# Optimization experiments

Measured on AMD Instinct MI355X. Metric: run time of the kernel, lower is better.

The kernel has to match this reference:

```python
import jax, jax.numpy as jnp
import numpy as np

NAMES = ['tempo', 'chord', 'barbeat', 'type', 'pitch', 'duration', 'velocity']
VOCABS = [56, 135, 18, 4, 87, 18, 25]
EMBS = [128, 256, 64, 32, 512, 128, 128]
B, S, D, H, L, FF = 2, 2048, 512, 8, 8, 2048
HD = D // H
EPS = 1e-6


def _layernorm(x, g, b):
    m = x.mean(-1, keepdims=True)
    v = ((x - m) ** 2).mean(-1, keepdims=True)
    return (x - m) / jnp.sqrt(v + 1e-5) * g + b


def _rope(x, cos, sin):
    x1, x2 = jnp.split(x, 2, -1)
    return x * cos + jnp.concatenate([-x2, x1], -1) * sin


def _causal_linear_attn(q, k, v):
    # kernelized causal linear attention: phi = elu + 1, cumulative-sum normalization
    q = jax.nn.elu(q) + 1.0
    k = jax.nn.elu(k) + 1.0
    kv = jnp.cumsum(jnp.einsum('bshd,bshm->bshdm', k, v), axis=1)  # [B,S,H,HD,HD]
    z = 1.0 / (jnp.einsum('bshd,bshd->bsh', q, jnp.cumsum(k, axis=1)) + EPS)
    return jnp.einsum('bshd,bshdm->bshm', q, kv) * z[..., None]


def _forward(inputs, target, emb_tables, in_W, in_b, Wq, bq, Wk, bk, Wv, bv, Wo, bo,
             ln1_g, ln1_b, ln2_g, ln2_b, W1, b1, W2, b2, norm_g, norm_b, pWs, pbs, catW, catb):
    # multi-field embedding, each scaled by sqrt(d_emb) (CPEmbedding)
    embs = [emb_tables[i][inputs[..., i]] * jnp.sqrt(jnp.float32(EMBS[i])) for i in range(7)]
    x = jnp.concatenate(embs, -1) @ in_W + in_b  # [B,S,D]
    # PositionalEncoding: original indexes pe at position seq_len -> single d_model vector
    div = jnp.exp(jnp.arange(0, D, 2, dtype=jnp.float32) * (-np.log(10000.0) / D))
    pe = jnp.zeros((D,), jnp.float32).at[0::2].set(jnp.sin(S * div)).at[1::2].set(jnp.cos(S * div))
    x = x + pe
    # rotary tables for head_dim
    inv_freq = 1.0 / (10000.0 ** (jnp.arange(0, HD, 2, dtype=jnp.float32) / HD))
    fr = jnp.arange(S, dtype=jnp.float32)[:, None] * inv_freq[None, :]
    ang = jnp.concatenate([fr, fr], -1)  # [S,HD]
    cos = jnp.cos(ang)[None, :, None, :]
    sin = jnp.sin(ang)[None, :, None, :]
    for l in range(L):
        q = (x @ Wq[l] + bq[l]).reshape(B, S, H, HD)
        k = (x @ Wk[l] + bk[l]).reshape(B, S, H, HD)
        v = (x @ Wv[l] + bv[l]).reshape(B, S, H, HD)
        q = _rope(q, cos, sin)
        k = _rope(k, cos, sin)
        a = _causal_linear_attn(q, k, v).reshape(B, S, D) @ Wo[l] + bo[l]
        x = x + a
        y = x = _layernorm(x, ln1_g[l], ln1_b[l])
        y = jax.nn.gelu(y @ W1[l] + b1[l], approximate=False) @ W2[l] + b2[l]
        x = _layernorm(x + y, ln2_g[l], ln2_b[l])
    x = _layernorm(x, norm_g, norm_b)
    # MultiProj with teacher-forced type embedding (target branch)
    emb_t = emb_tables[3][target[..., 3]] * jnp.sqrt(jnp.float32(EMBS[3]))
    proj_type = (x @ pWs[3] + pbs[3]) * jnp.sqrt(jnp.float32(VOCABS[3]))  # from pre-concat x
    xc = jnp.concatenate([x, emb_t], -1) @ catW + catb
    outs = []
    for i in range(7):
        if i == 3:
            outs.append(proj_type)
        else:
            outs.append((xc @ pWs[i] + pbs[i]) * jnp.sqrt(jnp.float32(VOCABS[i])))
    return jnp.concatenate(outs, -1)  # [B,S,sum(VOCABS)=343]


def setup_inputs():
    key = jax.random.key(0)
    kit = iter(jax.random.split(key, 64))
    s = 0.02
    d = {}
    d['inputs'] = jax.random.randint(next(kit), (B, S, 7), 0, 4)
    d['target'] = jax.random.randint(next(kit), (B, S, 7), 0, 4)
    for i, n in enumerate(NAMES):
        d['emb_' + n] = jax.random.normal(next(kit), (VOCABS[i], EMBS[i]), jnp.float32) * s
    E = sum(EMBS)
    d['in_W'] = jax.random.normal(next(kit), (E, D)) * s
    d['in_b'] = jnp.zeros((D,))
    for nm, sh in [('Wq', (L, D, D)), ('Wk', (L, D, D)), ('Wv', (L, D, D)), ('Wo', (L, D, D)), ('W1', (L, D, FF)), ('W2', (L, FF, D))]:
        d[nm] = jax.random.normal(next(kit), sh) * s
    for nm, sh in [('bq', (L, D)), ('bk', (L, D)), ('bv', (L, D)), ('bo', (L, D)), ('b1', (L, FF)), ('b2', (L, D)), ('ln1_b', (L, D)), ('ln2_b', (L, D)), ('norm_b', (D,)), ('catb', (D,))]:
        d[nm] = jnp.zeros(sh)
    d['ln1_g'] = jnp.ones((L, D))
    d['ln2_g'] = jnp.ones((L, D))
    d['norm_g'] = jnp.ones((D,))
    for i, n in enumerate(NAMES):
        d['pW_' + n] = jax.random.normal(next(kit), (D, VOCABS[i])) * s
        d['pb_' + n] = jnp.zeros((VOCABS[i],))
    d['catW'] = jax.random.normal(next(kit), (D + 32, D)) * s
    return d


def reference(inputs, target, emb_tempo, emb_chord, emb_barbeat, emb_type, emb_pitch, emb_duration, emb_velocity,
              in_W, in_b, Wq, bq, Wk, bk, Wv, bv, Wo, bo, ln1_g, ln1_b, ln2_g, ln2_b, W1, b1, W2, b2,
              norm_g, norm_b, pW_tempo, pb_tempo, pW_chord, pb_chord, pW_barbeat, pb_barbeat, pW_type, pb_type,
              pW_pitch, pb_pitch, pW_duration, pb_duration, pW_velocity, pb_velocity, catW, catb):
    emb_tables = [emb_tempo, emb_chord, emb_barbeat, emb_type, emb_pitch, emb_duration, emb_velocity]
    pWs = [pW_tempo, pW_chord, pW_barbeat, pW_type, pW_pitch, pW_duration, pW_velocity]
    pbs = [pb_tempo, pb_chord, pb_barbeat, pb_type, pb_pitch, pb_duration, pb_velocity]
    return _forward(inputs, target, emb_tables, in_W, in_b, Wq, bq, Wk, bk, Wv, bv, Wo, bo,
                    ln1_g, ln1_b, ln2_g, ln2_b, W1, b1, W2, b2, norm_g, norm_b, pWs, pbs, catW, catb)
```

## Files before the change

### kernel.cpp

```cpp
#include <hip/hip_runtime.h>
#include <math.h>

typedef unsigned short u16;
typedef short bf16x8 __attribute__((ext_vector_type(8)));
typedef float f32x4 __attribute__((ext_vector_type(4)));
typedef u16 u16x4 __attribute__((ext_vector_type(4)));
typedef u16 u16x8 __attribute__((ext_vector_type(8)));

#define NB 2
#define NS 2048
#define ND 512
#define NH 8
#define NHD 64
#define NL 8
#define NFF 2048
#define NM (NB*NS)
#define NE 1248
#define NEP 1280
#define NXC 576
#define CHK 64
#define NCH (NS/CHK)
#define QKVW 1536

__device__ inline float b2f(u16 u){ union{ unsigned int i; float f;} x; x.i = ((unsigned int)u)<<16; return x.f; }
__device__ inline u16 f2b(float f){ union{ float f; unsigned int i;} x; x.f=f; unsigned int r = x.i + 0x7fffu + ((x.i>>16)&1u); return (u16)(r>>16); }

__global__ void k_embed(const int* __restrict__ inp,
    const float* __restrict__ e0, const float* __restrict__ e1, const float* __restrict__ e2,
    const float* __restrict__ e3, const float* __restrict__ e4, const float* __restrict__ e5,
    const float* __restrict__ e6, u16* __restrict__ xe)
{
  int row = blockIdx.x;
  int i0 = inp[row*7+0], i1 = inp[row*7+1], i2 = inp[row*7+2], i3 = inp[row*7+3],
      i4 = inp[row*7+4], i5 = inp[row*7+5], i6 = inp[row*7+6];
  size_t base = (size_t)row*NEP;
  for (int c = threadIdx.x; c < NEP; c += 256){
    float val = 0.f;
    if      (c < 128)  val = e0[i0*128 + c]        * 11.3137084990f;
    else if (c < 384)  val = e1[i1*256 + (c-128)]  * 16.0f;
    else if (c < 448)  val = e2[i2*64  + (c-384)]  * 8.0f;
    else if (c < 480)  val = e3[i3*32  + (c-448)]  * 5.6568542495f;
    else if (c < 992)  val = e4[i4*512 + (c-480)]  * 22.6274169980f;
    else if (c < 1120) val = e5[i5*128 + (c-992)]  * 11.3137084990f;
    else if (c < NE)   val = e6[i6*128 + (c-1120)] * 11.3137084990f;
    xe[base + c] = f2b(val);
  }
}

__device__ inline void trans_tile(const float* __restrict__ W, u16* __restrict__ WT,
                                  int K, int N, int Kpad, int bx, int by){
  __shared__ float t[32][33];
  int tx = threadIdx.x & 31, ty = threadIdx.x >> 5;
  int k0 = by*32, n0 = bx*32;
  #pragma unroll
  for (int i=0;i<4;i++){
    int k = k0 + ty + i*8, n = n0 + tx;
    t[ty+i*8][tx] = (k<K && n<N) ? W[(size_t)k*N + n] : 0.f;
  }
  __syncthreads();
  #pragma unroll
  for (int i=0;i<4;i++){
    int n = n0 + ty + i*8, k = k0 + tx;
    if (n<N && k<Kpad) WT[(size_t)n*Kpad + k] = f2b(t[tx][ty+i*8]);
  }
}

__global__ void k_prepw(const float* __restrict__ Wq, const float* __restrict__ Wk,
                        const float* __restrict__ Wv, const float* __restrict__ Wo,
                        const float* __restrict__ in_W, const float* __restrict__ catW,
                        const float* __restrict__ W1, const float* __restrict__ W2,
                        u16* __restrict__ qkvoT, u16* __restrict__ inWT, u16* __restrict__ catWT,
                        u16* __restrict__ w1T, u16* __restrict__ w2T)
{
  int bid = blockIdx.x;
  if (bid < 8192){
    int z = bid >> 8, r = bid & 255;
    int l = z >> 2, s2 = z & 3;
    const float* W = (s2==0?Wq:s2==1?Wk:s2==2?Wv:Wo) + (size_t)l*ND*ND;
    trans_tile(W, qkvoT + (size_t)z*ND*ND, ND, ND, ND, r & 15, r >> 4);
  } else if (bid < 8832){
    int r = bid - 8192;
    trans_tile(in_W, inWT, NE, ND, NEP, r & 15, r >> 4);
  } else if (bid < 9120){
    int r = bid - 8832;
    trans_tile(catW, catWT, 544, ND, NXC, r & 15, r >> 4);
  } else {
    int r = bid - 9120;
    int l = r >> 11; int b2 = r & 2047;
    if (b2 < 1024) trans_tile(W1 + (size_t)l*ND*NFF, w1T + (size_t)l*ND*NFF, ND, NFF, ND, b2 & 63, b2 >> 6);
    else { b2 -= 1024; trans_tile(W2 + (size_t)l*NFF*ND, w2T + (size_t)l*NFF*ND, NFF, ND, NFF, b2 & 15, b2 >> 4); }
  }
}

__global__ void k_misc(float* __restrict__ rc, float* __restrict__ rs,
    const float* p0,const float* p1,const float* p2,const float* p3,
    const float* p4,const float* p5,const float* p6,
    const float* q0,const float* q1,const float* q2,const float* q3,
    const float* q4,const float* q5,const float* q6,
    u16* __restrict__ pwcT, float* __restrict__ pbc,
    u16* __restrict__ ptT, float* __restrict__ pbt,
    const float* __restrict__ bq, const float* __restrict__ bk, const float* __restrict__ bv,
    float* __restrict__ bqkv, const float* __restrict__ in_b, float* __restrict__ bias_in)
{
  int idx = blockIdx.x*256 + threadIdx.x;
  if (idx < NS*32){
    int s = idx >> 5, j = idx & 31;
    double inv = exp(-(double)(2*j) * log(10000.0) / (double)NHD);
    double ang = (double)s * inv;
    rc[idx] = (float)cos(ang);
    rs[idx] = (float)sin(ang);
  }
  const int off[8] = {0,56,191,209,213,300,318,343};
  {
    int col = idx >> 9, k = idx & 511;
    if (col < 384){
      u16 v = 0;
      if (col < 343){
        int f = 0;
        while (col >= off[f+1]) f++;
        int cc = col - off[f];
        int V = off[f+1]-off[f];
        const float* P = (f==0)?p0:(f==1)?p1:(f==2)?p2:(f==3)?p3:(f==4)?p4:(f==5)?p5:p6;
        v = f2b(P[(size_t)k*V + cc] * sqrtf((float)V));
      }
      pwcT[(size_t)col*512 + k] = v;
    }
    if (idx < 64*512){
      int n = idx >> 9;
      ptT[idx] = (n < 4) ? f2b(p3[(size_t)k*4 + n]*2.0f) : (u16)0;
    }
  }
  if (idx < 343){
    int c2 = idx, f = 0;
    while (c2 >= off[f+1]) f++;
    int cc = c2 - off[f]; int V = off[f+1]-off[f];
    const float* Q = (f==0)?q0:(f==1)?q1:(f==2)?q2:(f==3)?q3:(f==4)?q4:(f==5)?q5:q6;
    pbc[idx] = Q[cc]*sqrtf((float)V);
  }
  if (idx < 4) pbt[idx] = q3[idx]*2.0f;
  if (idx < NL*QKVW){
    int l = idx / QKVW, c = idx % QKVW;
    float v = (c < 512) ? bq[l*512 + c] : (c < 1024) ? bk[l*512 + c - 512] : bv[l*512 + c - 1024];
    bqkv[idx] = v;
  }
  if (idx < ND){
    double div = exp(-(double)(idx & ~1) * log(10000.0) / (double)ND);
    double ang = (double)NS * div;
    float pev = (idx & 1) ? (float)cos(ang) : (float)sin(ang);
    bias_in[idx] = in_b[idx] + pev;
  }
}

template<int ACT, int NT, int TM>
__global__ __launch_bounds__(256) void k_gemm(
    const u16* __restrict__ A, const u16* __restrict__ BT,
    const float* __restrict__ bias, float* __restrict__ Cf, u16* __restrict__ Cb,
    int N, int klen, int lda, int ldb, int ldc,
    int koff, float* __restrict__ Cf2,
    const float* __restrict__ rc, const float* __restrict__ rs)
{
  constexpr int MREP = TM/32;
  __shared__ u16 SH[TM*64 + NT*32*64];
  u16* As = SH;
  u16* Bs = SH + TM*64;
  int tid = threadIdx.x;
  int w = tid >> 6, lane = tid & 63;

  int kz = blockIdx.z;
  A  += (size_t)kz*koff;
  BT += (size_t)kz*koff;
  if (kz){ Cf = Cf2; bias = nullptr; }

  int nwg = gridDim.x*gridDim.y;
  int d = blockIdx.y*gridDim.x + blockIdx.x;
  int wl = ((nwg & 7) == 0) ? ((d & 7)*(nwg >> 3) + (d >> 3)) : d;
  int bx = wl % gridDim.x, by = wl / gridDim.x;
  int m0 = by*TM, n0 = bx*(NT*32);

  f32x4 acc[MREP][NT];
  #pragma unroll
  for (int m=0;m<MREP;m++)
    #pragma unroll
    for (int n=0;n<NT;n++) acc[m][n] = (f32x4){0.f,0.f,0.f,0.f};

  int lg = lane>>3;
  int cg = (lane&7) ^ lg;
  const u16* ag = A  + (size_t)(m0 + w*(TM/4) + lg)*lda + cg*8;
  const u16* bg = BT + (size_t)(n0 + w*(NT*8) + lg)*ldb + cg*8;
  int wr = (w>>1)*(TM/2), wc = (w&1)*(NT*16);
  int lr = lane & 15;
  int rx = lr & 7;
  int cb_ = lane >> 4;
  int g = lane >> 4;

  int nk = klen >> 6;
  for (int t = 0; t < nk; ++t){
    int k0 = t << 6;
    #pragma unroll
    for (int i=0;i<TM/32;i++)
      __builtin_amdgcn_global_load_lds(
        (__attribute__((address_space(1))) void*)(void*)(ag + (size_t)(i*8)*lda + k0),
        (__attribute__((address_space(3))) void*)(&As[(w*(TM/4) + i*8)*64]), 16, 0, 0);
    #pragma unroll
    for (int j=0;j<NT;j++)
      __builtin_amdgcn_global_load_lds(
        (__attribute__((address_space(1))) void*)(void*)(bg + (size_t)(j*8)*ldb + k0),
        (__attribute__((address_space(3))) void*)(&Bs[(w*(NT*8) + j*8)*64]), 16, 0, 0);
    __syncthreads();
    #pragma unroll
    for (int kk=0;kk<2;kk++){
      int gA = ((kk*4 + cb_) ^ rx) * 8;
      bf16x8 af[MREP], bfr[NT];
      #pragma unroll
      for (int m=0;m<MREP;m++) af[m]  = *(const bf16x8*)&As[(wr + m*16 + lr)*64 + gA];
      #pragma unroll
      for (int n=0;n<NT;n++)   bfr[n] = *(const bf16x8*)&Bs[(wc + n*16 + lr)*64 + gA];
      #pragma unroll
      for (int m=0;m<MREP;m++)
        #pragma unroll
        for (int n=0;n<NT;n++)
          acc[m][n] = __builtin_amdgcn_mfma_f32_16x16x32_bf16(af[m], bfr[n], acc[m][n], 0,0,0);
    }
    __syncthreads();
  }

  if (ACT == 2){
    float* Cs = (float*)SH;
    #pragma unroll
    for (int n=0;n<NT;n++){
      int col = wc + n*16 + lr;
      float bv = bias ? bias[n0 + col] : 0.f;
      #pragma unroll
      for (int m=0;m<MREP;m++)
        #pragma unroll
        for (int r=0;r<4;r++)
          Cs[(wr + m*16 + g*4 + r)*64 + col] = acc[m][n][r] + bv;
    }
    __syncthreads();
    if (n0 < 1024){
      #pragma unroll
      for (int i=0;i<8;i++){
        int p = tid + i*256;
        int row = p >> 5, j = p & 31;
        float a1 = Cs[row*64 + j], a2 = Cs[row*64 + j + 32];
        int s = (m0 + row) & (NS-1);
        float c = rc[s*32+j], sn = rs[s*32+j];
        float r1 = a1*c - a2*sn, r2 = a2*c + a1*sn;
        Cb[(size_t)(m0+row)*ldc + n0 + j]      = f2b((r1 > 0.f) ? r1+1.f : expf(r1));
        Cb[(size_t)(m0+row)*ldc + n0 + j + 32] = f2b((r2 > 0.f) ? r2+1.f : expf(r2));
      }
    } else {
      #pragma unroll
      for (int i=0;i<16;i++){
        int p = tid + i*256;
        int row = p >> 6, c2 = p & 63;
        Cb[(size_t)(m0+row)*ldc + n0 + c2] = f2b(Cs[row*64 + c2]);
      }
    }
    return;
  }

  #pragma unroll
  for (int n=0;n<NT;n++){
    int col = n0 + wc + n*16 + lr;
    if (col < N){
      float bv = bias ? bias[col] : 0.f;
      #pragma unroll
      for (int m=0;m<MREP;m++){
        #pragma unroll
        for (int r=0;r<4;r++){
          int row = m0 + wr + m*16 + g*4 + r;
          float v = acc[m][n][r] + bv;
          if (ACT==1) v = 0.5f*v*(1.f+erff(v*0.70710678118654752f));
          if (Cf) Cf[(size_t)row*ldc + col] = v;
          if (Cb) Cb[(size_t)row*ldc + col] = f2b(v);
        }
      }
    }
  }
}

__global__ __launch_bounds__(256) void k_att1(const u16* __restrict__ qkv, float* __restrict__ pref){
  int c = blockIdx.x, h = blockIdx.y, b = blockIdx.z;
  __shared__ u16 Kt[64*64];
  __shared__ u16 Vt[80*64];
  int tid = threadIdx.x;
  {
    int t = tid & 63, dseg = (tid>>6)*16;
    const u16* kg = qkv + ((size_t)(b*NS + c*CHK + t))*QKVW + 512 + h*NHD + dseg;
    u16x8 k0 = *(const u16x8*)kg;
    u16x8 k1 = *(const u16x8*)(kg+8);
    u16x8 v0 = *(const u16x8*)(kg+512);
    u16x8 v1 = *(const u16x8*)(kg+520);
    #pragma unroll
    for (int e=0;e<8;e++){
      int d0 = dseg+e, d1 = dseg+8+e;
      Kt[(d0*64+t) ^ ((d0&7)<<3)] = k0[e];
      Kt[(d1*64+t) ^ ((d1&7)<<3)] = k1[e];
      Vt[(d0*64+t) ^ ((d0&7)<<3)] = v0[e];
      Vt[(d1*64+t) ^ ((d1&7)<<3)] = v1[e];
    }
    if (tid < 64) Vt[4096 + tid] = 0x3F80;
    for (int e = tid; e < 15*64; e += 256){
      int r = 65 + (e>>6), tt = e&63;
      Vt[(r*64+tt) ^ ((r&7)<<3)] = 0;
    }
  }
  __syncthreads();
  int lane = tid & 63, w = tid >> 6;
  int lr = lane & 15, lk = (lane>>4)*8;
  f32x4 acc[5];
  #pragma unroll
  for (int i=0;i<5;i++) acc[i] = (f32x4){0.f,0.f,0.f,0.f};
  #pragma unroll
  for (int kk=0;kk<2;kk++){
    int mcol = w*16 + lr;
    bf16x8 bfrag = *(const bf16x8*)&Kt[(mcol*64 + kk*32 + lk) ^ ((mcol&7)<<3)];
    #pragma unroll
    for (int fr=0; fr<5; fr++){
      int arow = fr*16 + lr;
      bf16x8 afrag = *(const bf16x8*)&Vt[(arow*64 + kk*32 + lk) ^ ((arow&7)<<3)];
      acc[fr] = __builtin_amdgcn_mfma_f32_16x16x32_bf16(afrag, bfrag, acc[fr], 0,0,0);
    }
  }
  size_t base = (((size_t)(b*NH + h))*NCH + c)*5120;
  int g = lane>>4;
  #pragma unroll
  for (int fr=0; fr<5; fr++)
    #pragma unroll
    for (int r=0;r<4;r++)
      pref[base + (fr*16 + g*4 + r)*64 + w*16 + lr] = acc[fr][r];
}

__global__ __launch_bounds__(256) void k_att2(float* __restrict__ pref){
  int bh = blockIdx.y;
  int e = blockIdx.x*256 + threadIdx.x;
  size_t base = (size_t)bh*NCH*5120 + e;
  float v[NCH];
  #pragma unroll
  for (int c=0;c<NCH;c++) v[c] = pref[base + (size_t)c*5120];
  float run = 0.f;
  #pragma unroll
  for (int c=0;c<NCH;c++){ float t = v[c]; pref[base + (size_t)c*5120] = run; run += t; }
}

__global__ __launch_bounds__(256) void k_att3(const u16* __restrict__ qkv,
    const float* __restrict__ pref, u16* __restrict__ outa)
{
  int c = blockIdx.x, h = blockIdx.y, b = blockIdx.z;
  __shared__ u16 Qs[4096], Ks[4096];
  __shared__ u16 Vt[5120], Ps[5120];
  __shared__ float dens[64];
  u16* Sm = Ks;
  int tid = threadIdx.x;
  {
    int row = tid>>2, seg = (tid&3)*16;
    const u16* qg = qkv + ((size_t)(b*NS + c*CHK + row))*QKVW + h*NHD + seg;
    u16x8 q0 = *(const u16x8*)qg;
    u16x8 q1 = *(const u16x8*)(qg+8);
    u16x8 kk0 = *(const u16x8*)(qg+512);
    u16x8 kk1 = *(const u16x8*)(qg+520);
    int sw = (row&7)<<3;
    *(u16x8*)&Qs[(row*64+seg) ^ sw]     = q0;
    *(u16x8*)&Qs[(row*64+seg+8) ^ sw]   = q1;
    *(u16x8*)&Ks[(row*64+seg) ^ sw]     = kk0;
    *(u16x8*)&Ks[(row*64+seg+8) ^ sw]   = kk1;
  }
  {
    int t = tid&63, dseg = (tid>>6)*16;
    const u16* vg = qkv + ((size_t)(b*NS + c*CHK + t))*QKVW + 1024 + h*NHD + dseg;
    u16x8 v0 = *(const u16x8*)vg;
    u16x8 v1 = *(const u16x8*)(vg+8);
    #pragma unroll
    for (int e=0;e<8;e++){
      int d0=dseg+e, d1=dseg+8+e;
      Vt[(d0*64+t)^((d0&7)<<3)] = v0[e];
      Vt[(d1*64+t)^((d1&7)<<3)] = v1[e];
    }
    if (tid<64) Vt[4096+tid] = 0x3F80;
    for (int e=tid; e<15*64; e+=256){
      int r = 65+(e>>6), tt = e&63;
      Vt[(r*64+tt)^((r&7)<<3)] = 0;
    }
  }
  {
    size_t pb = (((size_t)(b*NH + h))*NCH + c)*5120;
    for (int e=tid; e<5120; e+=256){
      int row = e>>6, m = e&63;
      Ps[(row*64+m)^((row&7)<<3)] = f2b(pref[pb+e]);
    }
  }
  __syncthreads();
  int lane = tid&63, w = tid>>6;
  int lr = lane&15, lk = (lane>>4)*8, g = lane>>4;
  f32x4 sacc[4];
  #pragma unroll
  for (int i=0;i<4;i++) sacc[i] = (f32x4){0.f,0.f,0.f,0.f};
  int iq = w*16 + lr;
  #pragma unroll
  for (int kk=0;kk<2;kk++){
    bf16x8 bq = *(const bf16x8*)&Qs[(iq*64 + kk*32 + lk) ^ ((iq&7)<<3)];
    #pragma unroll
    for (int ft=0; ft<4; ft++){
      int tr = ft*16 + lr;
      bf16x8 ak = *(const bf16x8*)&Ks[(tr*64 + kk*32 + lk) ^ ((tr&7)<<3)];
      sacc[ft] = __builtin_amdgcn_mfma_f32_16x16x32_bf16(ak, bq, sacc[ft], 0,0,0);
    }
  }
  __syncthreads();
  #pragma unroll
  for (int ft=0; ft<4; ft++){
    int t0 = ft*16 + g*4;
    u16x4 pk;
    #pragma unroll
    for (int r=0;r<4;r++) pk[r] = f2b((t0+r <= iq) ? sacc[ft][r] : 0.f);
    *(u16x4*)&Sm[(iq*64 + t0) ^ ((iq&7)<<3)] = pk;
  }
  __syncthreads();
  f32x4 acc[5];
  #pragma unroll
  for (int i=0;i<5;i++) acc[i] = (f32x4){0.f,0.f,0.f,0.f};
  #pragma unroll
  for (int kk=0;kk<2;kk++){
    int sw = (iq&7)<<3;
    bf16x8 as = *(const bf16x8*)&Sm[(iq*64 + kk*32 + lk) ^ sw];
    bf16x8 aq = *(const bf16x8*)&Qs[(iq*64 + kk*32 + lk) ^ sw];
    #pragma unroll
    for (int c5=0;c5<5;c5++){
      int col = c5*16 + lr, sw2 = (col&7)<<3;
      bf16x8 bv = *(const bf16x8*)&Vt[(col*64 + kk*32 + lk) ^ sw2];
      bf16x8 bp = *(const bf16x8*)&Ps[(col*64 + kk*32 + lk) ^ sw2];
      acc[c5] = __builtin_amdgcn_mfma_f32_16x16x32_bf16(as, bv, acc[c5], 0,0,0);
      acc[c5] = __builtin_amdgcn_mfma_f32_16x16x32_bf16(aq, bp, acc[c5], 0,0,0);
    }
  }
  if (lr == 0){
    #pragma unroll
    for (int r=0;r<4;r++) dens[w*16 + g*4 + r] = acc[4][r];
  }
  __syncthreads();
  #pragma unroll
  for (int c5=0;c5<4;c5++){
    #pragma unroll
    for (int r=0;r<4;r++){
      int i = w*16 + g*4 + r;
      float z = 1.f/(dens[i] + 1e-6f);
      outa[((size_t)(b*NS + c*CHK + i))*ND + h*NHD + c5*16 + lr] = f2b(acc[c5][r]*z);
    }
  }
}

__global__ __launch_bounds__(256) void k_ln(const float* __restrict__ xin, const float* __restrict__ res,
    const float* __restrict__ res2, float* __restrict__ outx, u16* __restrict__ outb,
    const float* __restrict__ g, const float* __restrict__ bvec,
    const int* __restrict__ tgt, const float* __restrict__ embt, u16* __restrict__ xcb)
{
  int row = blockIdx.x, tid = threadIdx.x;
  size_t base = (size_t)row*ND;
  float v0 = xin[base+tid], v1 = xin[base+tid+256];
  if (res){ v0 += res[base+tid]; v1 += res[base+tid+256]; }
  if (res2){ v0 += res2[base+tid]; v1 += res2[base+tid+256]; }
  float s = v0+v1, ss2 = v0*v0 + v1*v1;
  #pragma unroll
  for (int o = 32; o >= 1; o >>= 1){
    s   += __shfl_down(s, o, 64);
    ss2 += __shfl_down(ss2, o, 64);
  }
  __shared__ float red[8];
  int wv = tid >> 6, ln = tid & 63;
  if (ln == 0){ red[wv] = s; red[4+wv] = ss2; }
  __syncthreads();
  float stot  = red[0]+red[1]+red[2]+red[3];
  float sstot = red[4]+red[5]+red[6]+red[7];
  float mean = stot * (1.0f/ND);
  float var  = sstot * (1.0f/ND) - mean*mean;
  float inv = 1.0f / sqrtf(var + 1e-5f);
  float o0 = (v0-mean)*inv*g[tid]     + bvec[tid];
  float o1 = (v1-mean)*inv*g[tid+256] + bvec[tid+256];
  outx[base+tid] = o0; outx[base+tid+256] = o1;
  if (outb){ outb[base+tid] = f2b(o0); outb[base+tid+256] = f2b(o1); }
  if (xcb){
    size_t xbse = (size_t)row*NXC;
    xcb[xbse+tid] = f2b(o0);
    xcb[xbse+tid+256] = f2b(o1);
    if (tid < 32){
      int id = tgt[row*7+3];
      xcb[xbse+512+tid] = f2b(embt[id*32+tid]*5.6568542495f);
      xcb[xbse+544+tid] = 0;
    }
  }
}

extern "C" void kernel_launch(void* const* d_in, const int* in_sizes, int n_in,
                              void* d_out, int out_size, void* d_ws, size_t ws_size,
                              hipStream_t stream)
{
  const int* inputs = (const int*)d_in[0];
  const int* target = (const int*)d_in[1];
  const float* emb[7];
  for (int i=0;i<7;i++) emb[i] = (const float*)d_in[2+i];
  const float* in_W  = (const float*)d_in[9];
  const float* in_b  = (const float*)d_in[10];
  const float* Wq = (const float*)d_in[11];
  const float* Wk = (const float*)d_in[12];
  const float* Wv = (const float*)d_in[13];
  const float* Wo = (const float*)d_in[14];
  const float* W1 = (const float*)d_in[15];
  const float* W2 = (const float*)d_in[16];
  const float* bq = (const float*)d_in[17];
  const float* bk = (const float*)d_in[18];
  const float* bv = (const float*)d_in[19];
  const float* bo = (const float*)d_in[20];
  const float* b1 = (const float*)d_in[21];
  const float* b2 = (const float*)d_in[22];
  const float* ln1_b = (const float*)d_in[23];
  const float* ln2_b = (const float*)d_in[24];
  const float* norm_b = (const float*)d_in[25];
  const float* catb   = (const float*)d_in[26];
  const float* ln1_g = (const float*)d_in[27];
  const float* ln2_g = (const float*)d_in[28];
  const float* norm_g = (const float*)d_in[29];
  const float* pW[7]; const float* pb[7];
  for (int i=0;i<7;i++){ pW[i]=(const float*)d_in[30+2*i]; pb[i]=(const float*)d_in[31+2*i]; }
  const float* catW = (const float*)d_in[44];
  float* outp = (float*)d_out;

  char* base = (char*)d_ws;
  size_t off = 0;
  auto alloc = [&](size_t bytes)->void*{ void* p = base + off; off += bytes; off = (off + 255) & ~(size_t)255; return p; };

  float* x    = (float*)alloc((size_t)NM*ND*4);
  u16*   xb   = (u16*)  alloc((size_t)NM*ND*2);
  u16*   qkvb = (u16*)  alloc((size_t)NM*QKVW*2);
  float* tb   = (float*)alloc((size_t)NM*ND*4);
  float* tb2  = (float*)alloc((size_t)NM*ND*4);
  u16*   ab   = (u16*)  alloc((size_t)NM*ND*2);
  u16*   hb   = (u16*)  alloc((size_t)NM*NFF*2);
  float* rc   = (float*)alloc((size_t)NS*32*4);
  float* rs   = (float*)alloc((size_t)NS*32*4);
  float* pref = (float*)alloc((size_t)NB*NH*NCH*5120*4);
  u16*  qkvoT = (u16*)  alloc((size_t)NL*4*ND*ND*2);
  u16*  w1T   = (u16*)  alloc((size_t)NL*NFF*ND*2);
  u16*  w2T   = (u16*)  alloc((size_t)NL*ND*NFF*2);
  u16*  inWT  = (u16*)  alloc((size_t)ND*NEP*2);
  u16*  catWT = (u16*)  alloc((size_t)ND*NXC*2);
  u16*  pwcT  = (u16*)  alloc((size_t)384*512*2);
  float* pbc  = (float*)alloc(344*4);
  u16*  ptT   = (u16*)  alloc((size_t)64*512*2);
  float* pbt  = (float*)alloc(4*4);
  float* bqkv = (float*)alloc((size_t)NL*QKVW*4);
  float* bias_in = (float*)alloc(ND*4);
  u16*  xeb = hb;
  u16*  xcb = hb;
  u16*  ocb = hb + (size_t)NM*NXC;

  k_prepw<<<25504, 256, 0, stream>>>(Wq, Wk, Wv, Wo, in_W, catW, W1, W2,
                                     qkvoT, inWT, catWT, w1T, w2T);
  k_misc<<<768, 256, 0, stream>>>(rc, rs,
      pW[0],pW[1],pW[2],pW[3],pW[4],pW[5],pW[6],
      pb[0],pb[1],pb[2],pb[3],pb[4],pb[5],pb[6],
      pwcT, pbc, ptT, pbt, bq, bk, bv, bqkv, in_b, bias_in);

  k_embed<<<NM, 256, 0, stream>>>(inputs, emb[0],emb[1],emb[2],emb[3],emb[4],emb[5],emb[6], xeb);
  k_gemm<0,2,64><<<dim3(8,64,1), 256, 0, stream>>>(xeb, inWT, bias_in, x, xb,
      ND, NEP, NEP, NEP, ND, 0, nullptr, nullptr, nullptr);

  dim3 agrid(NCH, NH, NB);
  for (int l = 0; l < NL; l++){
    const u16* woT = qkvoT + (size_t)(l*4+3)*ND*ND;
    k_gemm<2,2,64><<<dim3(24,64,1), 256, 0, stream>>>(xb, qkvoT + (size_t)l*4*ND*ND,
        bqkv + l*QKVW, nullptr, qkvb, QKVW, ND, ND, ND, QKVW, 0, nullptr, rc, rs);
    k_att1<<<agrid, 256, 0, stream>>>(qkvb, pref);
    k_att2<<<dim3(20,16), 256, 0, stream>>>(pref);
    k_att3<<<agrid, 256, 0, stream>>>(qkvb, pref, ab);
    k_gemm<0,2,64><<<dim3(8,64,2), 256, 0, stream>>>(ab, woT, bo + l*ND, tb, nullptr,
        ND, 256, ND, ND, ND, 256, tb2, nullptr, nullptr);
    k_ln<<<NM, 256, 0, stream>>>(x, tb, tb2, x, xb, ln1_g + l*ND, ln1_b + l*ND,
                                 nullptr, nullptr, nullptr);
    k_gemm<1,2,64><<<dim3(32,64,1), 256, 0, stream>>>(xb, w1T + (size_t)l*NFF*ND,
        b1 + l*NFF, nullptr, hb, NFF, ND, ND, ND, NFF, 0, nullptr, nullptr, nullptr);
    k_gemm<0,2,64><<<dim3(8,64,2), 256, 0, stream>>>(hb, w2T + (size_t)l*ND*NFF,
        b2 + l*ND, tb, nullptr, ND, 1024, NFF, NFF, ND, 1024, tb2, nullptr, nullptr);
    k_ln<<<NM, 256, 0, stream>>>(x, tb, tb2, x, xb, ln2_g + l*ND, ln2_b + l*ND,
                                 nullptr, nullptr, nullptr);
  }

  k_ln<<<NM, 256, 0, stream>>>(x, nullptr, nullptr, x, xb, norm_g, norm_b,
                               target, emb[3], xcb);

  k_gemm<0,2,64><<<dim3(8,64,1), 256, 0, stream>>>(xcb, catWT, catb, nullptr, ocb,
      ND, NXC, NXC, NXC, ND, 0, nullptr, nullptr, nullptr);
  k_gemm<0,2,64><<<dim3(6,64,1), 256, 0, stream>>>(ocb, pwcT, pbc, outp, nullptr,
      343, ND, ND, ND, 343, 0, nullptr, nullptr, nullptr);
  k_gemm<0,2,64><<<dim3(1,64,1), 256, 0, stream>>>(xb, ptT, pbt, outp + 209, nullptr,
      4, ND, ND, ND, 343, 0, nullptr, nullptr, nullptr);
}
```

Baseline: 828.5 us.

## Double-buffer GEMM LDS staging, widen weight transposes, and store attention prefixes as bf16

The GEMM kernel now uses two LDS buffers and issues the global-to-LDS loads for the next K tile before computing on the current one, so load latency can overlap the MFMA work. The weight-transpose prep kernel moves from 32x32 float tiles to 128x128 tiles with float4 reads, 16-byte writes and a swizzled bf16 LDS buffer, which cuts the block count and the number of narrow memory transactions. k_att2 now writes the chunk-prefix KV state as pre-swizzled bf16, and k_att3 fetches Q, K and the prefix state with direct global_load_lds copies instead of converting float prefixes in registers. These changes double GEMM LDS use, which may lower occupancy, and depend on the existing loop-end barrier for correct buffer reuse.

```diff
diff --git a/kernel.cpp b/kernel.cpp
--- a/kernel.cpp
+++ b/kernel.cpp
@@ -24,6 +24,10 @@
 
 __device__ inline float b2f(u16 u){ union{ unsigned int i; float f;} x; x.i = ((unsigned int)u)<<16; return x.f; }
 __device__ inline u16 f2b(float f){ union{ float f; unsigned int i;} x; x.f=f; unsigned int r = x.i + 0x7fffu + ((x.i>>16)&1u); return (u16)(r>>16); }
+
+#define GLL(src, dst) __builtin_amdgcn_global_load_lds( \
+    (__attribute__((address_space(1))) void*)(void*)(src), \
+    (__attribute__((address_space(3))) void*)(dst), 16, 0, 0)
 
 __global__ void k_embed(const int* __restrict__ inp,
     const float* __restrict__ e0, const float* __restrict__ e1, const float* __restrict__ e2,
@@ -47,21 +51,33 @@
   }
 }
 
-__device__ inline void trans_tile(const float* __restrict__ W, u16* __restrict__ WT,
-                                  int K, int N, int Kpad, int bx, int by){
-  __shared__ float t[32][33];
-  int tx = threadIdx.x & 31, ty = threadIdx.x >> 5;
-  int k0 = by*32, n0 = bx*32;
-  #pragma unroll
-  for (int i=0;i<4;i++){
-    int k = k0 + ty + i*8, n = n0 + tx;
-    t[ty+i*8][tx] = (k<K && n<N) ? W[(size_t)k*N + n] : 0.f;
-  }
-  __syncthreads();
-  #pragma unroll
-  for (int i=0;i<4;i++){
-    int n = n0 + ty + i*8, k = k0 + tx;
-    if (n<N && k<Kpad) WT[(size_t)n*Kpad + k] = f2b(t[tx][ty+i*8]);
+__device__ inline void trans_tile128(const float* __restrict__ W, u16* __restrict__ WT,
+                                     int K, int N, int Kpad, int bx, int by){
+  __shared__ u16 t[128*128];
+  int tid = threadIdx.x;
+  int k0 = by*128, n0 = bx*128;
+  int c = tid & 31, sub = tid >> 5;
+  #pragma unroll
+  for (int p=0;p<16;p++){
+    int kl = p*8 + sub;
+    int k = k0 + kl;
+    float4 v = {0.f,0.f,0.f,0.f};
+    if (k < K) v = *(const float4*)(W + (size_t)k*N + n0 + c*4);
+    #pragma unroll
+    for (int i=0;i<4;i++){
+      int n = c*4 + i;
+      int g = (kl>>3) ^ (n & 15);
+      t[n*128 + g*8 + (kl&7)] = f2b(((const float*)&v)[i]);
+    }
+  }
+  __syncthreads();
+  int kg = tid & 15, nsub = tid >> 4;
+  #pragma unroll
+  for (int p=0;p<8;p++){
+    int nl = p*16 + nsub;
+    int k = k0 + kg*8;
+    if (k < Kpad)
+      *(u16x8*)(WT + (size_t)(n0+nl)*Kpad + k) = *(const u16x8*)&t[nl*128 + ((kg ^ (nl&15))<<3)];
   }
 }
 
@@ -73,22 +89,25 @@
                         u16* __restrict__ w1T, u16* __restrict__ w2T)
 {
   int bid = blockIdx.x;
-  if (bid < 8192){
-    int z = bid >> 8, r = bid & 255;
+  if (bid < 512){
+    int z = bid >> 4, r = bid & 15;
     int l = z >> 2, s2 = z & 3;
     const float* W = (s2==0?Wq:s2==1?Wk:s2==2?Wv:Wo) + (size_t)l*ND*ND;
-    trans_tile(W, qkvoT + (size_t)z*ND*ND, ND, ND, ND, r & 15, r >> 4);
-  } else if (bid < 8832){
-    int r = bid - 8192;
-    trans_tile(in_W, inWT, NE, ND, NEP, r & 15, r >> 4);
-  } else if (bid < 9120){
-    int r = bid - 8832;
-    trans_tile(catW, catWT, 544, ND, NXC, r & 15, r >> 4);
+    trans_tile128(W, qkvoT + (size_t)z*ND*ND, ND, ND, ND, r & 3, r >> 2);
+  } else if (bid < 552){
+    int r = bid - 512;
+    trans_tile128(in_W, inWT, NE, ND, NEP, r & 3, r >> 2);
+  } else if (bid < 572){
+    int r = bid - 552;
+    trans_tile128(catW, catWT, 544, ND, NXC, r & 3, r >> 2);
+  } else if (bid < 1084){
+    int r = bid - 572;
+    int l = r >> 6; int rr = r & 63;
+    trans_tile128(W1 + (size_t)l*ND*NFF, w1T + (size_t)l*ND*NFF, ND, NFF, ND, rr & 15, rr >> 4);
   } else {
-    int r = bid - 9120;
-    int l = r >> 11; int b2 = r & 2047;
-    if (b2 < 1024) trans_tile(W1 + (size_t)l*ND*NFF, w1T + (size_t)l*ND*NFF, ND, NFF, ND, b2 & 63, b2 >> 6);
-    else { b2 -= 1024; trans_tile(W2 + (size_t)l*NFF*ND, w2T + (size_t)l*NFF*ND, NFF, ND, NFF, b2 & 15, b2 >> 4); }
+    int r = bid - 1084;
+    int l = r >> 6; int rr = r & 63;
+    trans_tile128(W2 + (size_t)l*NFF*ND, w2T + (size_t)l*ND*NFF, NFF, ND, NFF, rr & 3, rr >> 2);
   }
 }
 
@@ -160,9 +179,8 @@
     const float* __restrict__ rc, const float* __restrict__ rs)
 {
   constexpr int MREP = TM/32;
-  __shared__ u16 SH[TM*64 + NT*32*64];
-  u16* As = SH;
-  u16* Bs = SH + TM*64;
+  constexpr int BUFSZ = TM*64 + NT*32*64;
+  __shared__ u16 SH[2*BUFSZ];
   int tid = threadIdx.x;
   int w = tid >> 6, lane = tid & 63;
 
@@ -193,20 +211,25 @@
   int cb_ = lane >> 4;
   int g = lane >> 4;
 
+  auto STAGE = [&](int buf, int k0){
+    u16* As = SH + buf*BUFSZ;
+    u16* Bs = As + TM*64;
+    #pragma unroll
+    for (int i=0;i<TM/32;i++)
+      GLL(ag + (size_t)(i*8)*lda + k0, &As[(w*(TM/4) + i*8)*64]);
+    #pragma unroll
+    for (int j=0;j<NT;j++)
+      GLL(bg + (size_t)(j*8)*ldb + k0, &Bs[(w*(NT*8) + j*8)*64]);
+  };
+
   int nk = klen >> 6;
+  STAGE(0, 0);
+  __syncthreads();
   for (int t = 0; t < nk; ++t){
-    int k0 = t << 6;
-    #pragma unroll
-    for (int i=0;i<TM/32;i++)
-      __builtin_amdgcn_global_load_lds(
-        (__attribute__((address_space(1))) void*)(void*)(ag + (size_t)(i*8)*lda + k0),
-        (__attribute__((address_space(3))) void*)(&As[(w*(TM/4) + i*8)*64]), 16, 0, 0);
-    #pragma unroll
-    for (int j=0;j<NT;j++)
-      __builtin_amdgcn_global_load_lds(
-        (__attribute__((address_space(1))) void*)(void*)(bg + (size_t)(j*8)*ldb + k0),
-        (__attribute__((address_space(3))) void*)(&Bs[(w*(NT*8) + j*8)*64]), 16, 0, 0);
-    __syncthreads();
+    int cur = t & 1;
+    if (t+1 < nk) STAGE(cur^1, (t+1) << 6);
+    const u16* As = SH + cur*BUFSZ;
+    const u16* Bs = As + TM*64;
     #pragma unroll
     for (int kk=0;kk<2;kk++){
       int gA = ((kk*4 + cb_) ^ rx) * 8;
@@ -332,20 +355,22 @@
       pref[base + (fr*16 + g*4 + r)*64 + w*16 + lr] = acc[fr][r];
 }
 
-__global__ __launch_bounds__(256) void k_att2(float* __restrict__ pref){
+__global__ __launch_bounds__(256) void k_att2(const float* __restrict__ pref, u16* __restrict__ prefb){
   int bh = blockIdx.y;
   int e = blockIdx.x*256 + threadIdx.x;
   size_t base = (size_t)bh*NCH*5120 + e;
+  int se = e ^ (((e>>6)&7)<<3);
+  size_t sb = (size_t)bh*NCH*5120 + se;
   float v[NCH];
   #pragma unroll
   for (int c=0;c<NCH;c++) v[c] = pref[base + (size_t)c*5120];
   float run = 0.f;
   #pragma unroll
-  for (int c=0;c<NCH;c++){ float t = v[c]; pref[base + (size_t)c*5120] = run; run += t; }
+  for (int c=0;c<NCH;c++){ prefb[sb + (size_t)c*5120] = f2b(run); run += v[c]; }
 }
 
 __global__ __launch_bounds__(256) void k_att3(const u16* __restrict__ qkv,
-    const float* __restrict__ pref, u16* __restrict__ outa)
+    const u16* __restrict__ prefb, u16* __restrict__ outa)
 {
   int c = blockIdx.x, h = blockIdx.y, b = blockIdx.z;
   __shared__ u16 Qs[4096], Ks[4096];
@@ -353,18 +378,21 @@
   __shared__ float dens[64];
   u16* Sm = Ks;
   int tid = threadIdx.x;
+  int lane = tid & 63, w = tid >> 6;
   {
-    int row = tid>>2, seg = (tid&3)*16;
-    const u16* qg = qkv + ((size_t)(b*NS + c*CHK + row))*QKVW + h*NHD + seg;
-    u16x8 q0 = *(const u16x8*)qg;
-    u16x8 q1 = *(const u16x8*)(qg+8);
-    u16x8 kk0 = *(const u16x8*)(qg+512);
-    u16x8 kk1 = *(const u16x8*)(qg+520);
-    int sw = (row&7)<<3;
-    *(u16x8*)&Qs[(row*64+seg) ^ sw]     = q0;
-    *(u16x8*)&Qs[(row*64+seg+8) ^ sw]   = q1;
-    *(u16x8*)&Ks[(row*64+seg) ^ sw]     = kk0;
-    *(u16x8*)&Ks[(row*64+seg+8) ^ sw]   = kk1;
+    int r8 = lane >> 3;
+    int gsw = (lane & 7) ^ r8;
+    const u16* qbase = qkv + ((size_t)(b*NS + c*CHK))*QKVW + h*NHD + gsw*8;
+    #pragma unroll
+    for (int half = 0; half < 2; half++){
+      int rbase = w*16 + half*8;
+      const u16* src = qbase + (size_t)(rbase + r8)*QKVW;
+      GLL(src,       &Qs[rbase*64]);
+      GLL(src + 512, &Ks[rbase*64]);
+    }
+    const u16* pb = prefb + (((size_t)(b*NH + h))*NCH + c)*5120 + lane*8;
+    for (int ch = w; ch < 10; ch += 4)
+      GLL(pb + ch*512, &Ps[ch*512]);
   }
   {
     int t = tid&63, dseg = (tid>>6)*16;
@@ -383,15 +411,7 @@
       Vt[(r*64+tt)^((r&7)<<3)] = 0;
     }
   }
-  {
-    size_t pb = (((size_t)(b*NH + h))*NCH + c)*5120;
-    for (int e=tid; e<5120; e+=256){
-      int row = e>>6, m = e&63;
-      Ps[(row*64+m)^((row&7)<<3)] = f2b(pref[pb+e]);
-    }
-  }
-  __syncthreads();
-  int lane = tid&63, w = tid>>6;
+  __syncthreads();
   int lr = lane&15, lk = (lane>>4)*8, g = lane>>4;
   f32x4 sacc[4];
   #pragma unroll
@@ -539,6 +559,7 @@
   float* rc   = (float*)alloc((size_t)NS*32*4);
   float* rs   = (float*)alloc((size_t)NS*32*4);
   float* pref = (float*)alloc((size_t)NB*NH*NCH*5120*4);
+  u16*  prefb = (u16*)  alloc((size_t)NB*NH*NCH*5120*2);
   u16*  qkvoT = (u16*)  alloc((size_t)NL*4*ND*ND*2);
   u16*  w1T   = (u16*)  alloc((size_t)NL*NFF*ND*2);
   u16*  w2T   = (u16*)  alloc((size_t)NL*ND*NFF*2);
@@ -554,8 +575,8 @@
   u16*  xcb = hb;
   u16*  ocb = hb + (size_t)NM*NXC;
 
-  k_prepw<<<25504, 256, 0, stream>>>(Wq, Wk, Wv, Wo, in_W, catW, W1, W2,
-                                     qkvoT, inWT, catWT, w1T, w2T);
+  k_prepw<<<1596, 256, 0, stream>>>(Wq, Wk, Wv, Wo, in_W, catW, W1, W2,
+                                    qkvoT, inWT, catWT, w1T, w2T);
   k_misc<<<768, 256, 0, stream>>>(rc, rs,
       pW[0],pW[1],pW[2],pW[3],pW[4],pW[5],pW[6],
       pb[0],pb[1],pb[2],pb[3],pb[4],pb[5],pb[6],
@@ -571,8 +592,8 @@
     k_gemm<2,2,64><<<dim3(24,64,1), 256, 0, stream>>>(xb, qkvoT + (size_t)l*4*ND*ND,
         bqkv + l*QKVW, nullptr, qkvb, QKVW, ND, ND, ND, QKVW, 0, nullptr, rc, rs);
     k_att1<<<agrid, 256, 0, stream>>>(qkvb, pref);
-    k_att2<<<dim3(20,16), 256, 0, stream>>>(pref);
-    k_att3<<<agrid, 256, 0, stream>>>(qkvb, pref, ab);
+    k_att2<<<dim3(20,16), 256, 0, stream>>>(pref, prefb);
+    k_att3<<<agrid, 256, 0, stream>>>(qkvb, prefb, ab);
     k_gemm<0,2,64><<<dim3(8,64,2), 256, 0, stream>>>(ab, woT, bo + l*ND, tb, nullptr,
         ND, 256, ND, ND, ND, 256, tb2, nullptr, nullptr);
     k_ln<<<NM, 256, 0, stream>>>(x, tb, tb2, x, xb, ln1_g + l*ND, ln1_b + l*ND,
```

Result: no change. 833.2 us (+0.6%).
